# Optimization experiments

Measured on AMD Instinct MI355X. Metric: run time of the kernel, lower is better.

Reference implementation:

```python
import jax, jax.numpy as jnp
import numpy as np
from jax import lax

N, B, H, E = 50, 1024, 256, 256
FEA, SF = 8, 5
C_TANH = 10.0  # tanh_exploration, use_tanh=True for pointer


def setup_inputs() -> dict:
    key = jax.random.key(0)
    ks = iter(jax.random.split(key, 40))
    def rn(shape):
        return jax.random.normal(next(ks), shape, dtype=jnp.float32)
    def up(shape):
        s = 1.0 / np.sqrt(shape[-1])
        return jax.random.uniform(next(ks), shape, minval=-s, maxval=s, dtype=jnp.float32)
    inp = {
        'start_fea': rn((B, SF)),
        'decoder_input': rn((B, E)),
        'embedded_inputs': rn((N, B, E)),
        'hidden_h': rn((B, H)),
        'hidden_c': rn((B, H)),
        'context': rn((N, B, H)),
        'V': rn((B, N, FEA)),
        'V_reach_mask': jnp.zeros((B, N), dtype=bool),
        # LSTMCell (pointer decoder)
        'lstm_w_ih': up((4 * H, E)), 'lstm_w_hh': up((4 * H, H)),
        'lstm_b_ih': up((4 * H,)), 'lstm_b_hh': up((4 * H,)),
        # pointer attention
        'ptr_wq': up((H, H)), 'ptr_bq': up((H,)),
        'ptr_wr': up((H, H)), 'ptr_br': up((H,)), 'ptr_v': up((H,)),
        # glimpse attention
        'glp_wq': up((H, H)), 'glp_bq': up((H,)),
        'glp_wr': up((H, H)), 'glp_br': up((H,)), 'glp_v': up((H,)),
        # eta branch
        'fn_w': up((H, SF)),
        'eta_w_ih': up((4 * H, H)), 'eta_w_hh': up((4 * H, H)),
        'eta_b_ih': up((4 * H,)), 'eta_b_hh': up((4 * H,)),
        'eta_lin_w': up((1, 2 * H)), 'eta_lin_b': up((1,)),
    }
    return inp


def _lstm_cell(x, h, c, wi, wh, bi, bh):
    z = x @ wi.T + bi + h @ wh.T + bh
    i, f, g, o = jnp.split(z, 4, axis=1)  # torch chunk order i,f,g,o
    c2 = jax.nn.sigmoid(f) * c + jax.nn.sigmoid(i) * jnp.tanh(g)
    return jax.nn.sigmoid(o) * jnp.tanh(c2), c2


def _mask_modify(m):
    # if a row is all True, un-mask its last column
    return m.at[:, -1].set(jnp.where(m.all(axis=1), False, m[:, -1]))


def reference(start_fea, decoder_input, embedded_inputs, hidden_h, hidden_c,
              context, V, V_reach_mask,
              lstm_w_ih, lstm_w_hh, lstm_b_ih, lstm_b_hh,
              ptr_wq, ptr_bq, ptr_wr, ptr_br, ptr_v,
              glp_wq, glp_bq, glp_wr, glp_br, glp_v,
              fn_w, eta_w_ih, eta_w_hh, eta_b_ih, eta_b_hh,
              eta_lin_w, eta_lin_b):
    n_steps, bsz = embedded_inputs.shape[0], embedded_inputs.shape[1]
    barange = jnp.arange(bsz)
    # project_ref is a 1x1 conv over fixed context -> precompute once: [B,H,N]
    e_ptr = jnp.einsum('nbh,gh->bgn', context, ptr_wr) + ptr_br[None, :, None]
    e_glp = jnp.einsum('nbh,gh->bgn', context, glp_wr) + glp_br[None, :, None]

    def attn_logits(q_in, e, wq, bq, v):
        q = q_in @ wq.T + bq  # [B,H]
        return jnp.einsum('h,bhn->bn', v, jnp.tanh(q[:, :, None] + e))

    first_node = start_fea @ fn_w.T  # [B,H], no bias
    he, ce = _lstm_cell(first_node, hidden_h, hidden_c, eta_w_ih, eta_w_hh, eta_b_ih, eta_b_hh)
    mask0 = _mask_modify(V_reach_mask)

    def step(carry, step_i):
        h, c, mask, idxs, dec_in, heh, cec, last_node, cur_eta = carry
        upd = _mask_modify(mask.at[barange, idxs].set(True))
        logit_mask = jnp.where(step_i == 0, mask, upd)
        # pointer LSTM step
        h, c = _lstm_cell(dec_in, h, c, lstm_w_ih, lstm_w_hh, lstm_b_ih, lstm_b_hh)
        g_l = h
        # one glimpse (n_glimpses=1, mask_glimpses=True, use_tanh=False)
        u = attn_logits(g_l, e_glp, glp_wq, glp_bq, glp_v)
        u = jnp.where(logit_mask, -jnp.inf, u)
        g_l = jnp.einsum('bhn,bn->bh', e_glp, jax.nn.softmax(u, axis=1))
        # pointer (use_tanh=True, C=10, mask_logits=True)
        u = attn_logits(g_l, e_ptr, ptr_wq, ptr_bq, ptr_v)
        logits = jnp.where(logit_mask, -jnp.inf, C_TANH * jnp.tanh(u))
        log_p = jax.nn.log_softmax(logits, axis=1)  # [B,N]
        new_idxs = jnp.argmax(log_p, axis=1)  # greedy decode
        # eta branch
        cur_node = context[new_idxs, barange]  # [B,H]
        heh, cec = _lstm_cell(cur_node, heh, cec, eta_w_ih, eta_w_hh, eta_b_ih, eta_b_hh)
        eta = jnp.concatenate([last_node, cur_node], axis=1) @ eta_lin_w.T + eta_lin_b  # [B,1]
        cur_eta = cur_eta + eta
        dec_in2 = embedded_inputs[new_idxs, barange]  # [B,E]
        new_carry = (h, c, logit_mask, new_idxs, dec_in2, heh, cec, cur_node, cur_eta)
        return new_carry, (log_p, new_idxs, cur_eta[:, 0])

    init = (hidden_h, hidden_c, mask0, jnp.zeros((bsz,), jnp.int32), decoder_input,
            he, ce, first_node, jnp.zeros((bsz, 1), jnp.float32))
    _, (log_ps, sels, etas) = lax.scan(step, init, jnp.arange(n_steps))
    # stack along step dim -> [B, N, ...]
    return log_ps.transpose(1, 0, 2), sels.T, etas.T
```

## Files before the change

kernel.cpp:

```cpp
#include <hip/hip_runtime.h>
#include <hip/hip_bf16.h>

#define NSTEP 50
#define BSZ   1024
#define HD    256
#define RPB   4
#define NEG_INF (-__builtin_inff())

#define OFF_SEL ((size_t)BSZ * NSTEP * NSTEP)
#define OFF_ETA (OFF_SEL + (size_t)BSZ * NSTEP)

__device__ __forceinline__ float sigf(float x)      { return 1.f / (1.f + __expf(-x)); }
__device__ __forceinline__ float tanh_fast(float x) { return 1.f - 2.f / (__expf(2.f * x) + 1.f); }

__device__ __forceinline__ float wave_sum(float v) {
#pragma unroll
  for (int o = 1; o < 64; o <<= 1) v += __shfl_xor(v, o);
  return v;
}
__device__ __forceinline__ float wave_max(float v) {
#pragma unroll
  for (int o = 1; o < 64; o <<= 1) v = fmaxf(v, __shfl_xor(v, o));
  return v;
}

__global__ __launch_bounds__(256) void init_kernel(
    const float* __restrict__ w_ih, const float* __restrict__ w_hh,
    const float* __restrict__ b_ih, const float* __restrict__ b_hh,
    const float* __restrict__ glp_wq, const float* __restrict__ ptr_wq,
    float* __restrict__ wT2, float* __restrict__ bc,
    float* __restrict__ wqTg, float* __restrict__ wqTp)
{
  const int bid = blockIdx.x, tid = threadIdx.x;
  if (bid < 512) {
    const int k = bid;
    const float* src = (k < 256) ? (w_ih + k) : (w_hh + (k - 256));
#pragma unroll
    for (int g = 0; g < 4; ++g)
      wT2[(size_t)k * 1024 + tid * 4 + g] = src[(size_t)(g * 256 + tid) * 256];
  } else if (bid < 516) {
    const int j = (bid - 512) * 256 + tid;
    bc[j] = b_ih[j] + b_hh[j];
  } else {
    const int k = bid - 516;
    wqTg[(size_t)k * 256 + tid] = glp_wq[(size_t)tid * 256 + k];
    wqTp[(size_t)k * 256 + tid] = ptr_wq[(size_t)tid * 256 + k];
  }
}

__global__ __launch_bounds__(256) void e_kernel(
    const float* __restrict__ context,
    const float* __restrict__ glp_wr, const float* __restrict__ glp_br,
    const float* __restrict__ ptr_wr, const float* __restrict__ ptr_br,
    float* __restrict__ e_glp, float* __restrict__ e_ptr)
{
  __shared__ float ctx_lds[32][256];
  const int tid = threadIdx.x;
  const int n   = blockIdx.x >> 5;
  const int b0  = (blockIdx.x & 31) << 5;
  const float* src = context + ((size_t)n * BSZ + b0) * HD;
  for (int i = tid; i < 32 * 64; i += 256) {
    const int row = i >> 6, k4 = (i & 63) << 2;
    *(float4*)&ctx_lds[row][k4] = *(const float4*)&src[row * HD + k4];
  }
  __syncthreads();
  const int g  = tid;
  const float bg = glp_br[g], bp = ptr_br[g];
  for (int rg = 0; rg < 2; ++rg) {
    float ag[16], ap[16];
#pragma unroll
    for (int i = 0; i < 16; ++i) { ag[i] = 0.f; ap[i] = 0.f; }
    for (int k = 0; k < 256; k += 4) {
      float4 wg = *(const float4*)&glp_wr[g * HD + k];
      float4 wp = *(const float4*)&ptr_wr[g * HD + k];
#pragma unroll
      for (int i = 0; i < 16; ++i) {
        float4 a = *(const float4*)&ctx_lds[rg * 16 + i][k];
        ag[i] += a.x * wg.x + a.y * wg.y + a.z * wg.z + a.w * wg.w;
        ap[i] += a.x * wp.x + a.y * wp.y + a.z * wp.z + a.w * wp.w;
      }
    }
#pragma unroll
    for (int i = 0; i < 16; ++i) {
      const int b = b0 + rg * 16 + i;
      e_glp[((size_t)b * NSTEP + n) * HD + g] = ag[i] + bg;
      e_ptr[((size_t)b * NSTEP + n) * HD + g] = ap[i] + bp;
    }
  }
}

__global__ __launch_bounds__(256) void zx_kernel(
    const float* __restrict__ embedded, const float* __restrict__ decoder_input,
    const float* __restrict__ wT2, float* __restrict__ zx)
{
  __shared__ float x_lds[32][256];
  const int tid = threadIdx.x;
  const int n   = blockIdx.x >> 5;
  const int b0  = (blockIdx.x & 31) << 5;
  const float* src = (n < NSTEP) ? (embedded + ((size_t)n * BSZ + b0) * HD)
                                 : (decoder_input + (size_t)b0 * HD);
  for (int i = tid; i < 32 * 64; i += 256) {
    const int row = i >> 6, k4 = (i & 63) << 2;
    *(float4*)&x_lds[row][k4] = *(const float4*)&src[row * HD + k4];
  }
  __syncthreads();
  const float* wp = wT2 + (tid << 2);
  for (int rg = 0; rg < 2; ++rg) {
    float4 acc[16];
#pragma unroll
    for (int i = 0; i < 16; ++i) acc[i] = make_float4(0.f, 0.f, 0.f, 0.f);
    for (int k = 0; k < 256; k += 4) {
      float4 w0 = *(const float4*)(wp + (size_t)(k + 0) * 1024);
      float4 w1 = *(const float4*)(wp + (size_t)(k + 1) * 1024);
      float4 w2 = *(const float4*)(wp + (size_t)(k + 2) * 1024);
      float4 w3 = *(const float4*)(wp + (size_t)(k + 3) * 1024);
#pragma unroll
      for (int i = 0; i < 16; ++i) {
        float4 a = *(const float4*)&x_lds[rg * 16 + i][k];
        acc[i].x += a.x * w0.x + a.y * w1.x + a.z * w2.x + a.w * w3.x;
        acc[i].y += a.x * w0.y + a.y * w1.y + a.z * w2.y + a.w * w3.y;
        acc[i].z += a.x * w0.z + a.y * w1.z + a.z * w2.z + a.w * w3.z;
        acc[i].w += a.x * w0.w + a.y * w1.w + a.z * w2.w + a.w * w3.w;
      }
    }
#pragma unroll
    for (int i = 0; i < 16; ++i)
      *(float4*)&zx[((size_t)n * BSZ + (b0 + rg * 16 + i)) * 1024 + (tid << 2)] = acc[i];
  }
}

template <int PRE>
__global__ __launch_bounds__(512) void dec_kernel(
    const float* __restrict__ start_fea,
    const float* __restrict__ decoder_input,
    const float* __restrict__ embedded,
    const float* __restrict__ hidden_h,
    const float* __restrict__ hidden_c,
    const float* __restrict__ context,
    const unsigned char* __restrict__ vmask,
    const float* __restrict__ glp_bq, const float* __restrict__ glp_v,
    const float* __restrict__ ptr_bq, const float* __restrict__ ptr_v,
    const float* __restrict__ fn_w,
    const float* __restrict__ eta_lw, const float* __restrict__ eta_lb,
    const float* __restrict__ wT2, const float* __restrict__ bc,
    const float* __restrict__ wqTg, const float* __restrict__ wqTp,
    const float* __restrict__ e_glp, const float* __restrict__ e_ptr,
    const float* __restrict__ zx,
    float* __restrict__ out)
{
  __shared__ float a_lds[RPB][512];
  __shared__ float z_lds[RPB][1024];
  __shared__ float u_lds[RPB][52];
  __shared__ unsigned char mask_lds[RPB][64];
  __shared__ float ms_lds[RPB][2][2];
  __shared__ int   idx_lds[RPB];
  __shared__ float red_lds[8][2];
  __shared__ float eta_lds[RPB];

  const int tid  = threadIdx.x;
  const int col  = tid & 255;
  const int hf   = tid >> 8;
  const int wav  = tid >> 6;
  const int lane = tid & 63;
  const int b0   = blockIdx.x * RPB;
  const int r2   = hf * 2;
  const int cwr  = wav >> 1;
  const int cwh  = wav & 1;
  const int n0   = cwh * 25;
  const int k0   = hf << 7;

  float c_reg[2], ln_reg[2];

#pragma unroll
  for (int i2 = 0; i2 < 2; ++i2) {
    const int r = r2 + i2, b = b0 + r;
    a_lds[r][256 + col] = hidden_h[(size_t)b * HD + col];
    if (!PRE) a_lds[r][col] = decoder_input[(size_t)b * HD + col];
    c_reg[i2] = hidden_c[(size_t)b * HD + col];
    float fn = 0.f;
#pragma unroll
    for (int k = 0; k < 5; ++k) fn += start_fea[b * 5 + k] * fn_w[col * 5 + k];
    ln_reg[i2] = fn;
  }
  if (tid < RPB * NSTEP) {
    const int r = tid / NSTEP, n = tid - r * NSTEP;
    mask_lds[r][n] = vmask[(size_t)(b0 + r) * NSTEP + n];
  }
  if (tid < RPB) { eta_lds[tid] = 0.f; idx_lds[tid] = NSTEP; }
  __syncthreads();
  if (tid < RPB) {
    bool all = true;
    for (int n = 0; n < NSTEP; ++n) all = all && (mask_lds[tid][n] != 0);
    if (all) mask_lds[tid][NSTEP - 1] = 0;
  }
  __syncthreads();

  const float bch0 = bc[col], bch1 = bc[col + 256], bch2 = bc[col + 512], bch3 = bc[col + 768];
  const float lw0 = eta_lw[col], lw1 = eta_lw[HD + col];
  const float etaB = eta_lb[0];
  const float4 v4g  = *(const float4*)&glp_v[lane << 2];
  const float4 v4p  = *(const float4*)&ptr_v[lane << 2];
  const float4 v4bg = *(const float4*)&glp_bq[lane << 2];
  const float4 v4bp = *(const float4*)&ptr_bq[lane << 2];
  const int j2 = tid * 2;

  for (int t = 0; t < NSTEP; ++t) {
    {
      float2 acc[RPB];
      if (PRE) {
#pragma unroll
        for (int i = 0; i < RPB; ++i)
          acc[i] = *(const float2*)&zx[((size_t)idx_lds[i] * BSZ + (b0 + i)) * 1024 + j2];
      } else {
#pragma unroll
        for (int i = 0; i < RPB; ++i) acc[i] = make_float2(0.f, 0.f);
      }
      const int K0 = PRE ? 256 : 0;
      for (int k = K0; k < 512; k += 4) {
        float4 a4[RPB];
#pragma unroll
        for (int i = 0; i < RPB; ++i) a4[i] = *(const float4*)&a_lds[i][k];
        float2 w0 = *(const float2*)&wT2[(size_t)(k + 0) * 1024 + j2];
        float2 w1 = *(const float2*)&wT2[(size_t)(k + 1) * 1024 + j2];
        float2 w2 = *(const float2*)&wT2[(size_t)(k + 2) * 1024 + j2];
        float2 w3 = *(const float2*)&wT2[(size_t)(k + 3) * 1024 + j2];
#pragma unroll
        for (int i = 0; i < RPB; ++i) {
          acc[i].x += a4[i].x * w0.x + a4[i].y * w1.x + a4[i].z * w2.x + a4[i].w * w3.x;
          acc[i].y += a4[i].x * w0.y + a4[i].y * w1.y + a4[i].z * w2.y + a4[i].w * w3.y;
        }
      }
#pragma unroll
      for (int i = 0; i < RPB; ++i) *(float2*)&z_lds[i][j2] = acc[i];
    }
    __syncthreads();
#pragma unroll
    for (int i2 = 0; i2 < 2; ++i2) {
      const int r = r2 + i2;
      const float4 z4 = *(const float4*)&z_lds[r][col << 2];
      const float zi = z4.x + bch0, zf = z4.y + bch1, zg = z4.z + bch2, zo = z4.w + bch3;
      const float cn = sigf(zf) * c_reg[i2] + sigf(zi) * tanh_fast(zg);
      c_reg[i2] = cn;
      a_lds[r][256 + col] = sigf(zo) * tanh_fast(cn);
    }
    __syncthreads();
    {
      float accB[RPB] = {0.f, 0.f, 0.f, 0.f};
      for (int k = k0; k < k0 + 128; k += 4) {
        float4 a4[RPB];
#pragma unroll
        for (int i = 0; i < RPB; ++i) a4[i] = *(const float4*)&a_lds[i][256 + k];
        const float w0 = wqTg[(size_t)(k + 0) * 256 + col];
        const float w1 = wqTg[(size_t)(k + 1) * 256 + col];
        const float w2 = wqTg[(size_t)(k + 2) * 256 + col];
        const float w3 = wqTg[(size_t)(k + 3) * 256 + col];
#pragma unroll
        for (int i = 0; i < RPB; ++i)
          accB[i] += a4[i].x * w0 + a4[i].y * w1 + a4[i].z * w2 + a4[i].w * w3;
      }
#pragma unroll
      for (int i = 0; i < RPB; ++i) z_lds[i][(hf << 8) + col] = accB[i];
    }
    __syncthreads();
    {
      const int r = cwr, b = b0 + r;
      float4 q4;
      {
        const float4 p0 = *(const float4*)&z_lds[r][lane << 2];
        const float4 p1 = *(const float4*)&z_lds[r][256 + (lane << 2)];
        q4 = make_float4(p0.x + p1.x + v4bg.x, p0.y + p1.y + v4bg.y,
                         p0.z + p1.z + v4bg.z, p0.w + p1.w + v4bg.w);
      }
      float m = NEG_INF, s = 0.f;
      float4 G = make_float4(0.f, 0.f, 0.f, 0.f);
      const float* eb = e_glp + (size_t)b * NSTEP * HD;
      for (int n = n0; n < n0 + 25; ++n) {
        if (mask_lds[r][n]) continue;
        const float4 e4 = *(const float4*)&eb[n * HD + (lane << 2)];
        float uu = v4g.x * tanh_fast(q4.x + e4.x) + v4g.y * tanh_fast(q4.y + e4.y)
                 + v4g.z * tanh_fast(q4.z + e4.z) + v4g.w * tanh_fast(q4.w + e4.w);
        uu = wave_sum(uu);
        if (uu > m) {
          const float sc = __expf(m - uu);
          s *= sc; G.x *= sc; G.y *= sc; G.z *= sc; G.w *= sc;
          m = uu;
        }
        const float p = __expf(uu - m);
        s += p;
        G.x += p * e4.x; G.y += p * e4.y; G.z += p * e4.z; G.w += p * e4.w;
      }
      if (lane == 0) { ms_lds[r][cwh][0] = m; ms_lds[r][cwh][1] = s; }
      __syncthreads();
      const float mo = ms_lds[r][cwh ^ 1][0], so = ms_lds[r][cwh ^ 1][1];
      const float mg = fmaxf(m, mo);
      const float Z  = s * __expf(m - mg) + so * __expf(mo - mg);
      const float sc = __expf(m - mg) / Z;
      G.x *= sc; G.y *= sc; G.z *= sc; G.w *= sc;
      *(float4*)&z_lds[r][512 + (cwh << 8) + (lane << 2)] = G;
    }
    __syncthreads();
    {
      float accE[RPB] = {0.f, 0.f, 0.f, 0.f};
      for (int k = k0; k < k0 + 128; k += 4) {
        float4 g4[RPB];
#pragma unroll
        for (int i = 0; i < RPB; ++i) {
          const float4 ga = *(const float4*)&z_lds[i][512 + k];
          const float4 gb = *(const float4*)&z_lds[i][768 + k];
          g4[i] = make_float4(ga.x + gb.x, ga.y + gb.y, ga.z + gb.z, ga.w + gb.w);
        }
        const float w0 = wqTp[(size_t)(k + 0) * 256 + col];
        const float w1 = wqTp[(size_t)(k + 1) * 256 + col];
        const float w2 = wqTp[(size_t)(k + 2) * 256 + col];
        const float w3 = wqTp[(size_t)(k + 3) * 256 + col];
#pragma unroll
        for (int i = 0; i < RPB; ++i)
          accE[i] += g4[i].x * w0 + g4[i].y * w1 + g4[i].z * w2 + g4[i].w * w3;
      }
#pragma unroll
      for (int i = 0; i < RPB; ++i) z_lds[i][(hf << 8) + col] = accE[i];
    }
    __syncthreads();
    {
      const int r = cwr, b = b0 + r;
      float4 q4;
      {
        const float4 p0 = *(const float4*)&z_lds[r][lane << 2];
        const float4 p1 = *(const float4*)&z_lds[r][256 + (lane << 2)];
        q4 = make_float4(p0.x + p1.x + v4bp.x, p0.y + p1.y + v4bp.y,
                         p0.z + p1.z + v4bp.z, p0.w + p1.w + v4bp.w);
      }
      const float* eb = e_ptr + (size_t)b * NSTEP * HD;
      for (int n = n0; n < n0 + 25; ++n) {
        const float4 e4 = *(const float4*)&eb[n * HD + (lane << 2)];
        float uu = v4p.x * tanh_fast(q4.x + e4.x) + v4p.y * tanh_fast(q4.y + e4.y)
                 + v4p.z * tanh_fast(q4.z + e4.z) + v4p.w * tanh_fast(q4.w + e4.w);
        uu = wave_sum(uu);
        if (lane == 0) u_lds[r][n] = uu;
      }
    }
    __syncthreads();
    if (wav < RPB) {
      const int r = wav, b = b0 + r;
      const bool mk = (lane < NSTEP) ? (mask_lds[r][lane] != 0) : true;
      const float lg = mk ? NEG_INF : (10.f * tanh_fast(u_lds[r][lane]));
      const float m  = wave_max(lg);
      const float ex = (lane < NSTEP) ? __expf(lg - m) : 0.f;
      const float ss = wave_sum(ex);
      const float ls = __logf(ss);
      if (lane < NSTEP)
        out[(size_t)b * (NSTEP * NSTEP) + (size_t)t * NSTEP + lane] =
            mk ? -1.0e30f : ((lg - m) - ls);
      float av = lg;
      int   ai = lane;
#pragma unroll
      for (int o = 1; o < 64; o <<= 1) {
        const float ov = __shfl_xor(av, o);
        const int   oi = __shfl_xor(ai, o);
        if (ov > av || (ov == av && oi < ai)) { av = ov; ai = oi; }
      }
      if (lane == 0) {
        idx_lds[r] = ai;
        out[OFF_SEL + (size_t)b * NSTEP + t] = (float)ai;
      }
    }
    __syncthreads();
    {
      float pr[2];
#pragma unroll
      for (int i2 = 0; i2 < 2; ++i2) {
        const int r = r2 + i2, b = b0 + r;
        const int ix = idx_lds[r];
        const float cur = context[((size_t)ix * BSZ + b) * HD + col];
        pr[i2] = ln_reg[i2] * lw0 + cur * lw1;
        ln_reg[i2] = cur;
        if (!PRE) a_lds[r][col] = embedded[((size_t)ix * BSZ + b) * HD + col];
      }
#pragma unroll
      for (int o = 1; o < 64; o <<= 1) {
        pr[0] += __shfl_xor(pr[0], o);
        pr[1] += __shfl_xor(pr[1], o);
      }
      if (lane == 0) { red_lds[wav][0] = pr[0]; red_lds[wav][1] = pr[1]; }
    }
    __syncthreads();
    if (tid < RPB) {
      const int r = tid, hfr = r >> 1, i2 = r & 1;
      const float s = red_lds[hfr * 4 + 0][i2] + red_lds[hfr * 4 + 1][i2]
                    + red_lds[hfr * 4 + 2][i2] + red_lds[hfr * 4 + 3][i2];
      const float ev = eta_lds[r] + s + etaB;
      eta_lds[r] = ev;
      out[OFF_ETA + (size_t)(b0 + r) * NSTEP + t] = ev;
      const int ix = idx_lds[r];
      mask_lds[r][ix] = 1;
      bool all = true;
      for (int n = 0; n < NSTEP; ++n) all = all && (mask_lds[r][n] != 0);
      if (all) mask_lds[r][NSTEP - 1] = 0;
    }
    __syncthreads();
  }
}

extern "C" void kernel_launch(void* const* d_in, const int* in_sizes, int n_in,
                              void* d_out, int out_size, void* d_ws, size_t ws_size,
                              hipStream_t stream) {
  const float* start_fea  = (const float*)d_in[0];
  const float* decoder_in = (const float*)d_in[1];
  const float* embedded   = (const float*)d_in[2];
  const float* hidden_h   = (const float*)d_in[3];
  const float* hidden_c   = (const float*)d_in[4];
  const float* context    = (const float*)d_in[5];
  const unsigned char* vmask = (const unsigned char*)d_in[7];
  const float* lstm_w_ih  = (const float*)d_in[8];
  const float* lstm_w_hh  = (const float*)d_in[9];
  const float* lstm_b_ih  = (const float*)d_in[10];
  const float* lstm_b_hh  = (const float*)d_in[11];
  const float* ptr_wq     = (const float*)d_in[12];
  const float* ptr_bq     = (const float*)d_in[13];
  const float* ptr_wr     = (const float*)d_in[14];
  const float* ptr_br     = (const float*)d_in[15];
  const float* ptr_v      = (const float*)d_in[16];
  const float* glp_wq     = (const float*)d_in[17];
  const float* glp_bq     = (const float*)d_in[18];
  const float* glp_wr     = (const float*)d_in[19];
  const float* glp_br     = (const float*)d_in[20];
  const float* glp_v      = (const float*)d_in[21];
  const float* fn_w       = (const float*)d_in[22];
  const float* eta_lw     = (const float*)d_in[27];
  const float* eta_lb     = (const float*)d_in[28];

  float* ws    = (float*)d_ws;
  float* e_glp = ws;
  float* e_ptr = e_glp + (size_t)BSZ * NSTEP * HD;
  float* wT2   = e_ptr + (size_t)BSZ * NSTEP * HD;
  float* bc    = wT2 + (size_t)512 * 1024;
  float* wqTg  = bc + 1024;
  float* wqTp  = wqTg + 65536;
  float* zx    = wqTp + 65536;

  const size_t need_pre =
      ((size_t)BSZ * NSTEP * HD * 2 + (size_t)512 * 1024 + 1024 + 2 * 65536 +
       (size_t)(NSTEP + 1) * BSZ * 1024) * sizeof(float);
  const bool pre = (ws_size >= need_pre);

  init_kernel<<<772, 256, 0, stream>>>(lstm_w_ih, lstm_w_hh, lstm_b_ih, lstm_b_hh,
                                       glp_wq, ptr_wq, wT2, bc, wqTg, wqTp);
  e_kernel<<<NSTEP * 32, 256, 0, stream>>>(context, glp_wr, glp_br, ptr_wr, ptr_br, e_glp, e_ptr);
  if (pre) {
    zx_kernel<<<(NSTEP + 1) * 32, 256, 0, stream>>>(embedded, decoder_in, wT2, zx);
    dec_kernel<1><<<BSZ / RPB, 512, 0, stream>>>(
        start_fea, decoder_in, embedded, hidden_h, hidden_c, context, vmask,
        glp_bq, glp_v, ptr_bq, ptr_v, fn_w, eta_lw, eta_lb,
        wT2, bc, wqTg, wqTp, e_glp, e_ptr, zx, (float*)d_out);
  } else {
    dec_kernel<0><<<BSZ / RPB, 512, 0, stream>>>(
        start_fea, decoder_in, embedded, hidden_h, hidden_c, context, vmask,
        glp_bq, glp_v, ptr_bq, ptr_v, fn_w, eta_lw, eta_lb,
        wT2, bc, wqTg, wqTp, e_glp, e_ptr, zx, (float*)d_out);
  }
}
```

Before: 5.281 ms.

## Halve rows per block and split attention across four waves per row

Reduces rows per block from 4 to 2, doubling the block count so more blocks run per CU, and adds a launch-bounds occupancy hint. Each row's attention over the 50 nodes is now split across four waves instead of two, using a four-way online-softmax merge. A separate q_lds buffer holds query projections. The aim is more parallelism and latency hiding, at the cost of half the weight reuse per load and more total L2 weight traffic.

Measured after the change: 5.995 ms. 13.5% more time.

```diff
diff --git a/kernel.cpp b/kernel.cpp
--- a/kernel.cpp
+++ b/kernel.cpp
@@ -4,7 +4,7 @@
 #define NSTEP 50
 #define BSZ   1024
 #define HD    256
-#define RPB   4
+#define RPB   2
 #define NEG_INF (-__builtin_inff())
 
 #define OFF_SEL ((size_t)BSZ * NSTEP * NSTEP)
@@ -130,7 +130,7 @@
 }
 
 template <int PRE>
-__global__ __launch_bounds__(512) void dec_kernel(
+__global__ __launch_bounds__(512, 4) void dec_kernel(
     const float* __restrict__ start_fea,
     const float* __restrict__ decoder_input,
     const float* __restrict__ embedded,
@@ -150,11 +150,12 @@
 {
   __shared__ float a_lds[RPB][512];
   __shared__ float z_lds[RPB][1024];
+  __shared__ float q_lds[RPB][512];
   __shared__ float u_lds[RPB][52];
   __shared__ unsigned char mask_lds[RPB][64];
-  __shared__ float ms_lds[RPB][2][2];
+  __shared__ float ms_lds[RPB][4][2];
   __shared__ int   idx_lds[RPB];
-  __shared__ float red_lds[8][2];
+  __shared__ float red_lds[8];
   __shared__ float eta_lds[RPB];
 
   const int tid  = threadIdx.x;
@@ -163,24 +164,24 @@
   const int wav  = tid >> 6;
   const int lane = tid & 63;
   const int b0   = blockIdx.x * RPB;
-  const int r2   = hf * 2;
-  const int cwr  = wav >> 1;
-  const int cwh  = wav & 1;
-  const int n0   = cwh * 25;
+  const int cr   = wav >> 2;
+  const int cq   = wav & 3;
+  const int n0   = cq * 13;
+  const int n1   = (cq == 3) ? NSTEP : (n0 + 13);
   const int k0   = hf << 7;
-
-  float c_reg[2], ln_reg[2];
-
-#pragma unroll
-  for (int i2 = 0; i2 < 2; ++i2) {
-    const int r = r2 + i2, b = b0 + r;
+  const int j2   = tid * 2;
+
+  float c_reg, ln_reg;
+
+  {
+    const int r = hf, b = b0 + r;
     a_lds[r][256 + col] = hidden_h[(size_t)b * HD + col];
     if (!PRE) a_lds[r][col] = decoder_input[(size_t)b * HD + col];
-    c_reg[i2] = hidden_c[(size_t)b * HD + col];
+    c_reg = hidden_c[(size_t)b * HD + col];
     float fn = 0.f;
 #pragma unroll
     for (int k = 0; k < 5; ++k) fn += start_fea[b * 5 + k] * fn_w[col * 5 + k];
-    ln_reg[i2] = fn;
+    ln_reg = fn;
   }
   if (tid < RPB * NSTEP) {
     const int r = tid / NSTEP, n = tid - r * NSTEP;
@@ -202,7 +203,6 @@
   const float4 v4p  = *(const float4*)&ptr_v[lane << 2];
   const float4 v4bg = *(const float4*)&glp_bq[lane << 2];
   const float4 v4bp = *(const float4*)&ptr_bq[lane << 2];
-  const int j2 = tid * 2;
 
   for (int t = 0; t < NSTEP; ++t) {
     {
@@ -220,10 +220,10 @@
         float4 a4[RPB];
 #pragma unroll
         for (int i = 0; i < RPB; ++i) a4[i] = *(const float4*)&a_lds[i][k];
-        float2 w0 = *(const float2*)&wT2[(size_t)(k + 0) * 1024 + j2];
-        float2 w1 = *(const float2*)&wT2[(size_t)(k + 1) * 1024 + j2];
-        float2 w2 = *(const float2*)&wT2[(size_t)(k + 2) * 1024 + j2];
-        float2 w3 = *(const float2*)&wT2[(size_t)(k + 3) * 1024 + j2];
+        const float2 w0 = *(const float2*)&wT2[(size_t)(k + 0) * 1024 + j2];
+        const float2 w1 = *(const float2*)&wT2[(size_t)(k + 1) * 1024 + j2];
+        const float2 w2 = *(const float2*)&wT2[(size_t)(k + 2) * 1024 + j2];
+        const float2 w3 = *(const float2*)&wT2[(size_t)(k + 3) * 1024 + j2];
 #pragma unroll
         for (int i = 0; i < RPB; ++i) {
           acc[i].x += a4[i].x * w0.x + a4[i].y * w1.x + a4[i].z * w2.x + a4[i].w * w3.x;
@@ -234,18 +234,16 @@
       for (int i = 0; i < RPB; ++i) *(float2*)&z_lds[i][j2] = acc[i];
     }
     __syncthreads();
-#pragma unroll
-    for (int i2 = 0; i2 < 2; ++i2) {
-      const int r = r2 + i2;
-      const float4 z4 = *(const float4*)&z_lds[r][col << 2];
+    {
+      const float4 z4 = *(const float4*)&z_lds[hf][col << 2];
       const float zi = z4.x + bch0, zf = z4.y + bch1, zg = z4.z + bch2, zo = z4.w + bch3;
-      const float cn = sigf(zf) * c_reg[i2] + sigf(zi) * tanh_fast(zg);
-      c_reg[i2] = cn;
-      a_lds[r][256 + col] = sigf(zo) * tanh_fast(cn);
-    }
-    __syncthreads();
-    {
-      float accB[RPB] = {0.f, 0.f, 0.f, 0.f};
+      const float cn = sigf(zf) * c_reg + sigf(zi) * tanh_fast(zg);
+      c_reg = cn;
+      a_lds[hf][256 + col] = sigf(zo) * tanh_fast(cn);
+    }
+    __syncthreads();
+    {
+      float accB[RPB] = {0.f, 0.f};
       for (int k = k0; k < k0 + 128; k += 4) {
         float4 a4[RPB];
 #pragma unroll
@@ -259,22 +257,22 @@
           accB[i] += a4[i].x * w0 + a4[i].y * w1 + a4[i].z * w2 + a4[i].w * w3;
       }
 #pragma unroll
-      for (int i = 0; i < RPB; ++i) z_lds[i][(hf << 8) + col] = accB[i];
-    }
-    __syncthreads();
-    {
-      const int r = cwr, b = b0 + r;
+      for (int i = 0; i < RPB; ++i) q_lds[i][(hf << 8) + col] = accB[i];
+    }
+    __syncthreads();
+    {
+      const int r = cr, b = b0 + r;
       float4 q4;
       {
-        const float4 p0 = *(const float4*)&z_lds[r][lane << 2];
-        const float4 p1 = *(const float4*)&z_lds[r][256 + (lane << 2)];
+        const float4 p0 = *(const float4*)&q_lds[r][lane << 2];
+        const float4 p1 = *(const float4*)&q_lds[r][256 + (lane << 2)];
         q4 = make_float4(p0.x + p1.x + v4bg.x, p0.y + p1.y + v4bg.y,
                          p0.z + p1.z + v4bg.z, p0.w + p1.w + v4bg.w);
       }
       float m = NEG_INF, s = 0.f;
       float4 G = make_float4(0.f, 0.f, 0.f, 0.f);
       const float* eb = e_glp + (size_t)b * NSTEP * HD;
-      for (int n = n0; n < n0 + 25; ++n) {
+      for (int n = n0; n < n1; ++n) {
         if (mask_lds[r][n]) continue;
         const float4 e4 = *(const float4*)&eb[n * HD + (lane << 2)];
         float uu = v4g.x * tanh_fast(q4.x + e4.x) + v4g.y * tanh_fast(q4.y + e4.y)
@@ -289,25 +287,31 @@
         s += p;
         G.x += p * e4.x; G.y += p * e4.y; G.z += p * e4.z; G.w += p * e4.w;
       }
-      if (lane == 0) { ms_lds[r][cwh][0] = m; ms_lds[r][cwh][1] = s; }
+      if (lane == 0) { ms_lds[r][cq][0] = m; ms_lds[r][cq][1] = s; }
       __syncthreads();
-      const float mo = ms_lds[r][cwh ^ 1][0], so = ms_lds[r][cwh ^ 1][1];
-      const float mg = fmaxf(m, mo);
-      const float Z  = s * __expf(m - mg) + so * __expf(mo - mg);
+      float mg = NEG_INF;
+#pragma unroll
+      for (int q = 0; q < 4; ++q) mg = fmaxf(mg, ms_lds[r][q][0]);
+      float Z = 0.f;
+#pragma unroll
+      for (int q = 0; q < 4; ++q) Z += ms_lds[r][q][1] * __expf(ms_lds[r][q][0] - mg);
       const float sc = __expf(m - mg) / Z;
       G.x *= sc; G.y *= sc; G.z *= sc; G.w *= sc;
-      *(float4*)&z_lds[r][512 + (cwh << 8) + (lane << 2)] = G;
-    }
-    __syncthreads();
-    {
-      float accE[RPB] = {0.f, 0.f, 0.f, 0.f};
+      *(float4*)&z_lds[r][(cq << 8) + (lane << 2)] = G;
+    }
+    __syncthreads();
+    {
+      float accE[RPB] = {0.f, 0.f};
       for (int k = k0; k < k0 + 128; k += 4) {
         float4 g4[RPB];
 #pragma unroll
         for (int i = 0; i < RPB; ++i) {
-          const float4 ga = *(const float4*)&z_lds[i][512 + k];
-          const float4 gb = *(const float4*)&z_lds[i][768 + k];
-          g4[i] = make_float4(ga.x + gb.x, ga.y + gb.y, ga.z + gb.z, ga.w + gb.w);
+          const float4 g0 = *(const float4*)&z_lds[i][k];
+          const float4 g1 = *(const float4*)&z_lds[i][256 + k];
+          const float4 g2 = *(const float4*)&z_lds[i][512 + k];
+          const float4 g3 = *(const float4*)&z_lds[i][768 + k];
+          g4[i] = make_float4(g0.x + g1.x + g2.x + g3.x, g0.y + g1.y + g2.y + g3.y,
+                              g0.z + g1.z + g2.z + g3.z, g0.w + g1.w + g2.w + g3.w);
         }
         const float w0 = wqTp[(size_t)(k + 0) * 256 + col];
         const float w1 = wqTp[(size_t)(k + 1) * 256 + col];
@@ -318,20 +322,20 @@
           accE[i] += g4[i].x * w0 + g4[i].y * w1 + g4[i].z * w2 + g4[i].w * w3;
       }
 #pragma unroll
-      for (int i = 0; i < RPB; ++i) z_lds[i][(hf << 8) + col] = accE[i];
-    }
-    __syncthreads();
-    {
-      const int r = cwr, b = b0 + r;
+      for (int i = 0; i < RPB; ++i) q_lds[i][(hf << 8) + col] = accE[i];
+    }
+    __syncthreads();
+    {
+      const int r = cr, b = b0 + r;
       float4 q4;
       {
-        const float4 p0 = *(const float4*)&z_lds[r][lane << 2];
-        const float4 p1 = *(const float4*)&z_lds[r][256 + (lane << 2)];
+        const float4 p0 = *(const float4*)&q_lds[r][lane << 2];
+        const float4 p1 = *(const float4*)&q_lds[r][256 + (lane << 2)];
         q4 = make_float4(p0.x + p1.x + v4bp.x, p0.y + p1.y + v4bp.y,
                          p0.z + p1.z + v4bp.z, p0.w + p1.w + v4bp.w);
       }
       const float* eb = e_ptr + (size_t)b * NSTEP * HD;
-      for (int n = n0; n < n0 + 25; ++n) {
+      for (int n = n0; n < n1; ++n) {
         const float4 e4 = *(const float4*)&eb[n * HD + (lane << 2)];
         float uu = v4p.x * tanh_fast(q4.x + e4.x) + v4p.y * tanh_fast(q4.y + e4.y)
                  + v4p.z * tanh_fast(q4.z + e4.z) + v4p.w * tanh_fast(q4.w + e4.w);
@@ -366,28 +370,20 @@
     }
     __syncthreads();
     {
-      float pr[2];
-#pragma unroll
-      for (int i2 = 0; i2 < 2; ++i2) {
-        const int r = r2 + i2, b = b0 + r;
-        const int ix = idx_lds[r];
-        const float cur = context[((size_t)ix * BSZ + b) * HD + col];
-        pr[i2] = ln_reg[i2] * lw0 + cur * lw1;
-        ln_reg[i2] = cur;
-        if (!PRE) a_lds[r][col] = embedded[((size_t)ix * BSZ + b) * HD + col];
-      }
-#pragma unroll
-      for (int o = 1; o < 64; o <<= 1) {
-        pr[0] += __shfl_xor(pr[0], o);
-        pr[1] += __shfl_xor(pr[1], o);
-      }
-      if (lane == 0) { red_lds[wav][0] = pr[0]; red_lds[wav][1] = pr[1]; }
+      const int r = hf, b = b0 + r;
+      const int ix = idx_lds[r];
+      const float cur = context[((size_t)ix * BSZ + b) * HD + col];
+      float pr = ln_reg * lw0 + cur * lw1;
+      ln_reg = cur;
+      if (!PRE) a_lds[r][col] = embedded[((size_t)ix * BSZ + b) * HD + col];
+      pr = wave_sum(pr);
+      if (lane == 0) red_lds[wav] = pr;
     }
     __syncthreads();
     if (tid < RPB) {
-      const int r = tid, hfr = r >> 1, i2 = r & 1;
-      const float s = red_lds[hfr * 4 + 0][i2] + red_lds[hfr * 4 + 1][i2]
-                    + red_lds[hfr * 4 + 2][i2] + red_lds[hfr * 4 + 3][i2];
+      const int r = tid;
+      const float s = red_lds[r * 4 + 0] + red_lds[r * 4 + 1]
+                    + red_lds[r * 4 + 2] + red_lds[r * 4 + 3];
       const float ev = eta_lds[r] + s + etaB;
       eta_lds[r] = ev;
       out[OFF_ETA + (size_t)(b0 + r) * NSTEP + t] = ev;
```

## Transpose attention projections to per-node layout and parallelize attention over nodes

Applied to the files above, without the earlier changes.

Replaces the e_kernel with a per-batch et_kernel that stores the reference projections transposed as [B,H,N] and pre-scaled by 2, so the tanh folds into a single exp. In the decoder, each lane now handles one node and loops over the hidden dimension, replacing per-node wave reductions and the online softmax with one masked softmax and a separate weighted-sum pass. It also drops the precomputed zx input projection and computes the full 512-wide LSTM matmul every step. This trades extra per-step matmul work and strided global reads of the transposed projections for fewer cross-lane reductions and less serialization.

After: 9.690 ms. 83.5% more time.

```diff
diff --git a/kernel.cpp b/kernel.cpp
--- a/kernel.cpp
+++ b/kernel.cpp
@@ -48,88 +48,36 @@
   }
 }
 
-__global__ __launch_bounds__(256) void e_kernel(
+__global__ __launch_bounds__(256) void et_kernel(
     const float* __restrict__ context,
-    const float* __restrict__ glp_wr, const float* __restrict__ glp_br,
-    const float* __restrict__ ptr_wr, const float* __restrict__ ptr_br,
-    float* __restrict__ e_glp, float* __restrict__ e_ptr)
+    const float* __restrict__ wr, const float* __restrict__ br,
+    float* __restrict__ et)
 {
-  __shared__ float ctx_lds[32][256];
-  const int tid = threadIdx.x;
-  const int n   = blockIdx.x >> 5;
-  const int b0  = (blockIdx.x & 31) << 5;
-  const float* src = context + ((size_t)n * BSZ + b0) * HD;
-  for (int i = tid; i < 32 * 64; i += 256) {
-    const int row = i >> 6, k4 = (i & 63) << 2;
-    *(float4*)&ctx_lds[row][k4] = *(const float4*)&src[row * HD + k4];
+  __shared__ float c_lds[50][260];
+  const int b = blockIdx.x, tid = threadIdx.x;
+  for (int i = tid; i < 50 * 256; i += 256) {
+    const int n = i >> 8, k = i & 255;
+    c_lds[n][k] = context[((size_t)n * BSZ + b) * HD + k];
   }
   __syncthreads();
-  const int g  = tid;
-  const float bg = glp_br[g], bp = ptr_br[g];
-  for (int rg = 0; rg < 2; ++rg) {
-    float ag[16], ap[16];
-#pragma unroll
-    for (int i = 0; i < 16; ++i) { ag[i] = 0.f; ap[i] = 0.f; }
-    for (int k = 0; k < 256; k += 4) {
-      float4 wg = *(const float4*)&glp_wr[g * HD + k];
-      float4 wp = *(const float4*)&ptr_wr[g * HD + k];
-#pragma unroll
-      for (int i = 0; i < 16; ++i) {
-        float4 a = *(const float4*)&ctx_lds[rg * 16 + i][k];
-        ag[i] += a.x * wg.x + a.y * wg.y + a.z * wg.z + a.w * wg.w;
-        ap[i] += a.x * wp.x + a.y * wp.y + a.z * wp.z + a.w * wp.w;
-      }
-    }
-#pragma unroll
-    for (int i = 0; i < 16; ++i) {
-      const int b = b0 + rg * 16 + i;
-      e_glp[((size_t)b * NSTEP + n) * HD + g] = ag[i] + bg;
-      e_ptr[((size_t)b * NSTEP + n) * HD + g] = ap[i] + bp;
-    }
-  }
-}
-
-__global__ __launch_bounds__(256) void zx_kernel(
-    const float* __restrict__ embedded, const float* __restrict__ decoder_input,
-    const float* __restrict__ wT2, float* __restrict__ zx)
-{
-  __shared__ float x_lds[32][256];
-  const int tid = threadIdx.x;
-  const int n   = blockIdx.x >> 5;
-  const int b0  = (blockIdx.x & 31) << 5;
-  const float* src = (n < NSTEP) ? (embedded + ((size_t)n * BSZ + b0) * HD)
-                                 : (decoder_input + (size_t)b0 * HD);
-  for (int i = tid; i < 32 * 64; i += 256) {
-    const int row = i >> 6, k4 = (i & 63) << 2;
-    *(float4*)&x_lds[row][k4] = *(const float4*)&src[row * HD + k4];
-  }
-  __syncthreads();
-  const float* wp = wT2 + (tid << 2);
-  for (int rg = 0; rg < 2; ++rg) {
-    float4 acc[16];
-#pragma unroll
-    for (int i = 0; i < 16; ++i) acc[i] = make_float4(0.f, 0.f, 0.f, 0.f);
-    for (int k = 0; k < 256; k += 4) {
-      float4 w0 = *(const float4*)(wp + (size_t)(k + 0) * 1024);
-      float4 w1 = *(const float4*)(wp + (size_t)(k + 1) * 1024);
-      float4 w2 = *(const float4*)(wp + (size_t)(k + 2) * 1024);
-      float4 w3 = *(const float4*)(wp + (size_t)(k + 3) * 1024);
-#pragma unroll
-      for (int i = 0; i < 16; ++i) {
-        float4 a = *(const float4*)&x_lds[rg * 16 + i][k];
-        acc[i].x += a.x * w0.x + a.y * w1.x + a.z * w2.x + a.w * w3.x;
-        acc[i].y += a.x * w0.y + a.y * w1.y + a.z * w2.y + a.w * w3.y;
-        acc[i].z += a.x * w0.z + a.y * w1.z + a.z * w2.z + a.w * w3.z;
-        acc[i].w += a.x * w0.w + a.y * w1.w + a.z * w2.w + a.w * w3.w;
-      }
-    }
-#pragma unroll
-    for (int i = 0; i < 16; ++i)
-      *(float4*)&zx[((size_t)n * BSZ + (b0 + rg * 16 + i)) * 1024 + (tid << 2)] = acc[i];
-  }
-}
-
-template <int PRE>
+  float acc[50];
+#pragma unroll
+  for (int n = 0; n < 50; ++n) acc[n] = 0.f;
+  const float* wrh = wr + (size_t)tid * HD;
+  for (int k4 = 0; k4 < 64; ++k4) {
+    const float4 w4 = *(const float4*)&wrh[k4 * 4];
+#pragma unroll
+    for (int n = 0; n < 50; ++n) {
+      const float4 c4 = *(const float4*)&c_lds[n][k4 * 4];
+      acc[n] += c4.x * w4.x + c4.y * w4.y + c4.z * w4.z + c4.w * w4.w;
+    }
+  }
+  const float bb = br[tid];
+  float* dst = et + ((size_t)b * HD + tid) * NSTEP;
+#pragma unroll
+  for (int n = 0; n < 50; ++n) dst[n] = 2.f * (acc[n] + bb);
+}
+
 __global__ __launch_bounds__(512) void dec_kernel(
     const float* __restrict__ start_fea,
     const float* __restrict__ decoder_input,
@@ -144,15 +92,16 @@
     const float* __restrict__ eta_lw, const float* __restrict__ eta_lb,
     const float* __restrict__ wT2, const float* __restrict__ bc,
     const float* __restrict__ wqTg, const float* __restrict__ wqTp,
-    const float* __restrict__ e_glp, const float* __restrict__ e_ptr,
-    const float* __restrict__ zx,
+    const float* __restrict__ et_glp, const float* __restrict__ et_ptr,
     float* __restrict__ out)
 {
   __shared__ float a_lds[RPB][512];
   __shared__ float z_lds[RPB][1024];
-  __shared__ float u_lds[RPB][52];
+  __shared__ float qf_lds[RPB][256];
+  __shared__ float up_lds[RPB][2][64];
+  __shared__ float p_lds[RPB][64];
+  __shared__ float vv_lds[2][256];
   __shared__ unsigned char mask_lds[RPB][64];
-  __shared__ float ms_lds[RPB][2][2];
   __shared__ int   idx_lds[RPB];
   __shared__ float red_lds[8][2];
   __shared__ float eta_lds[RPB];
@@ -163,30 +112,30 @@
   const int wav  = tid >> 6;
   const int lane = tid & 63;
   const int b0   = blockIdx.x * RPB;
-  const int r2   = hf * 2;
-  const int cwr  = wav >> 1;
-  const int cwh  = wav & 1;
-  const int n0   = cwh * 25;
   const int k0   = hf << 7;
+  const int j2   = tid * 2;
+  const int cr   = wav >> 1;
+  const int ch   = wav & 1;
 
   float c_reg[2], ln_reg[2];
 
 #pragma unroll
-  for (int i2 = 0; i2 < 2; ++i2) {
-    const int r = r2 + i2, b = b0 + r;
+  for (int rr = 0; rr < 2; ++rr) {
+    const int r = hf * 2 + rr, b = b0 + r;
+    a_lds[r][col]       = decoder_input[(size_t)b * HD + col];
     a_lds[r][256 + col] = hidden_h[(size_t)b * HD + col];
-    if (!PRE) a_lds[r][col] = decoder_input[(size_t)b * HD + col];
-    c_reg[i2] = hidden_c[(size_t)b * HD + col];
+    c_reg[rr] = hidden_c[(size_t)b * HD + col];
     float fn = 0.f;
 #pragma unroll
     for (int k = 0; k < 5; ++k) fn += start_fea[b * 5 + k] * fn_w[col * 5 + k];
-    ln_reg[i2] = fn;
-  }
+    ln_reg[rr] = fn;
+  }
+  if (hf == 0) vv_lds[0][col] = glp_v[col]; else vv_lds[1][col] = ptr_v[col];
   if (tid < RPB * NSTEP) {
     const int r = tid / NSTEP, n = tid - r * NSTEP;
     mask_lds[r][n] = vmask[(size_t)(b0 + r) * NSTEP + n];
   }
-  if (tid < RPB) { eta_lds[tid] = 0.f; idx_lds[tid] = NSTEP; }
+  if (tid < RPB) { eta_lds[tid] = 0.f; idx_lds[tid] = 0; }
   __syncthreads();
   if (tid < RPB) {
     bool all = true;
@@ -198,32 +147,21 @@
   const float bch0 = bc[col], bch1 = bc[col + 256], bch2 = bc[col + 512], bch3 = bc[col + 768];
   const float lw0 = eta_lw[col], lw1 = eta_lw[HD + col];
   const float etaB = eta_lb[0];
-  const float4 v4g  = *(const float4*)&glp_v[lane << 2];
-  const float4 v4p  = *(const float4*)&ptr_v[lane << 2];
-  const float4 v4bg = *(const float4*)&glp_bq[lane << 2];
-  const float4 v4bp = *(const float4*)&ptr_bq[lane << 2];
-  const int j2 = tid * 2;
+  const float bqg = glp_bq[col], bqp = ptr_bq[col];
 
   for (int t = 0; t < NSTEP; ++t) {
     {
       float2 acc[RPB];
-      if (PRE) {
-#pragma unroll
-        for (int i = 0; i < RPB; ++i)
-          acc[i] = *(const float2*)&zx[((size_t)idx_lds[i] * BSZ + (b0 + i)) * 1024 + j2];
-      } else {
-#pragma unroll
-        for (int i = 0; i < RPB; ++i) acc[i] = make_float2(0.f, 0.f);
-      }
-      const int K0 = PRE ? 256 : 0;
-      for (int k = K0; k < 512; k += 4) {
+#pragma unroll
+      for (int i = 0; i < RPB; ++i) acc[i] = make_float2(0.f, 0.f);
+      for (int k = 0; k < 512; k += 4) {
         float4 a4[RPB];
 #pragma unroll
         for (int i = 0; i < RPB; ++i) a4[i] = *(const float4*)&a_lds[i][k];
-        float2 w0 = *(const float2*)&wT2[(size_t)(k + 0) * 1024 + j2];
-        float2 w1 = *(const float2*)&wT2[(size_t)(k + 1) * 1024 + j2];
-        float2 w2 = *(const float2*)&wT2[(size_t)(k + 2) * 1024 + j2];
-        float2 w3 = *(const float2*)&wT2[(size_t)(k + 3) * 1024 + j2];
+        const float2 w0 = *(const float2*)&wT2[(size_t)(k + 0) * 1024 + j2];
+        const float2 w1 = *(const float2*)&wT2[(size_t)(k + 1) * 1024 + j2];
+        const float2 w2 = *(const float2*)&wT2[(size_t)(k + 2) * 1024 + j2];
+        const float2 w3 = *(const float2*)&wT2[(size_t)(k + 3) * 1024 + j2];
 #pragma unroll
         for (int i = 0; i < RPB; ++i) {
           acc[i].x += a4[i].x * w0.x + a4[i].y * w1.x + a4[i].z * w2.x + a4[i].w * w3.x;
@@ -235,12 +173,12 @@
     }
     __syncthreads();
 #pragma unroll
-    for (int i2 = 0; i2 < 2; ++i2) {
-      const int r = r2 + i2;
+    for (int rr = 0; rr < 2; ++rr) {
+      const int r = hf * 2 + rr;
       const float4 z4 = *(const float4*)&z_lds[r][col << 2];
       const float zi = z4.x + bch0, zf = z4.y + bch1, zg = z4.z + bch2, zo = z4.w + bch3;
-      const float cn = sigf(zf) * c_reg[i2] + sigf(zi) * tanh_fast(zg);
-      c_reg[i2] = cn;
+      const float cn = sigf(zf) * c_reg[rr] + sigf(zi) * tanh_fast(zg);
+      c_reg[rr] = cn;
       a_lds[r][256 + col] = sigf(zo) * tanh_fast(cn);
     }
     __syncthreads();
@@ -262,41 +200,50 @@
       for (int i = 0; i < RPB; ++i) z_lds[i][(hf << 8) + col] = accB[i];
     }
     __syncthreads();
-    {
-      const int r = cwr, b = b0 + r;
-      float4 q4;
-      {
-        const float4 p0 = *(const float4*)&z_lds[r][lane << 2];
-        const float4 p1 = *(const float4*)&z_lds[r][256 + (lane << 2)];
-        q4 = make_float4(p0.x + p1.x + v4bg.x, p0.y + p1.y + v4bg.y,
-                         p0.z + p1.z + v4bg.z, p0.w + p1.w + v4bg.w);
-      }
-      float m = NEG_INF, s = 0.f;
-      float4 G = make_float4(0.f, 0.f, 0.f, 0.f);
-      const float* eb = e_glp + (size_t)b * NSTEP * HD;
-      for (int n = n0; n < n0 + 25; ++n) {
-        if (mask_lds[r][n]) continue;
-        const float4 e4 = *(const float4*)&eb[n * HD + (lane << 2)];
-        float uu = v4g.x * tanh_fast(q4.x + e4.x) + v4g.y * tanh_fast(q4.y + e4.y)
-                 + v4g.z * tanh_fast(q4.z + e4.z) + v4g.w * tanh_fast(q4.w + e4.w);
-        uu = wave_sum(uu);
-        if (uu > m) {
-          const float sc = __expf(m - uu);
-          s *= sc; G.x *= sc; G.y *= sc; G.z *= sc; G.w *= sc;
-          m = uu;
-        }
-        const float p = __expf(uu - m);
-        s += p;
-        G.x += p * e4.x; G.y += p * e4.y; G.z += p * e4.z; G.w += p * e4.w;
-      }
-      if (lane == 0) { ms_lds[r][cwh][0] = m; ms_lds[r][cwh][1] = s; }
-      __syncthreads();
-      const float mo = ms_lds[r][cwh ^ 1][0], so = ms_lds[r][cwh ^ 1][1];
-      const float mg = fmaxf(m, mo);
-      const float Z  = s * __expf(m - mg) + so * __expf(mo - mg);
-      const float sc = __expf(m - mg) / Z;
-      G.x *= sc; G.y *= sc; G.z *= sc; G.w *= sc;
-      *(float4*)&z_lds[r][512 + (cwh << 8) + (lane << 2)] = G;
+#pragma unroll
+    for (int rr = 0; rr < 2; ++rr) {
+      const int r = hf * 2 + rr;
+      qf_lds[r][col] = 2.f * (z_lds[r][col] + z_lds[r][256 + col] + bqg);
+    }
+    __syncthreads();
+    {
+      const int r = cr, b = b0 + r;
+      const float* et = et_glp + ((size_t)b * HD + (ch << 7)) * NSTEP + lane;
+      const float* qf = &qf_lds[r][ch << 7];
+      const float* vv = &vv_lds[0][ch << 7];
+      float u = 0.f;
+#pragma unroll 4
+      for (int h = 0; h < 128; ++h) {
+        const float x2 = qf[h] + et[h * NSTEP];
+        const float th = 1.f - 2.f / (__expf(x2) + 1.f);
+        u = fmaf(vv[h], th, u);
+      }
+      up_lds[r][ch][lane] = u;
+    }
+    __syncthreads();
+    if (wav < RPB) {
+      const int r = wav;
+      const bool mk = (lane < NSTEP) ? (mask_lds[r][lane] != 0) : true;
+      const float u = up_lds[r][0][lane] + up_lds[r][1][lane];
+      const float uv = mk ? NEG_INF : u;
+      const float m  = wave_max(uv);
+      const float ex = mk ? 0.f : __expf(uv - m);
+      const float ss = wave_sum(ex);
+      p_lds[r][lane] = 0.5f * (ex / ss);
+    }
+    __syncthreads();
+#pragma unroll
+    for (int rr = 0; rr < 2; ++rr) {
+      const int r = hf * 2 + rr, b = b0 + r;
+      const float2* eb = (const float2*)(et_glp + ((size_t)b * HD + col) * NSTEP);
+      float acc = 0.f;
+#pragma unroll
+      for (int q = 0; q < 25; ++q) {
+        const float2 e2 = eb[q];
+        const float2 p2 = *(const float2*)&p_lds[r][q * 2];
+        acc += e2.x * p2.x + e2.y * p2.y;
+      }
+      z_lds[r][col] = acc;
     }
     __syncthreads();
     {
@@ -304,11 +251,7 @@
       for (int k = k0; k < k0 + 128; k += 4) {
         float4 g4[RPB];
 #pragma unroll
-        for (int i = 0; i < RPB; ++i) {
-          const float4 ga = *(const float4*)&z_lds[i][512 + k];
-          const float4 gb = *(const float4*)&z_lds[i][768 + k];
-          g4[i] = make_float4(ga.x + gb.x, ga.y + gb.y, ga.z + gb.z, ga.w + gb.w);
-        }
+        for (int i = 0; i < RPB; ++i) g4[i] = *(const float4*)&z_lds[i][k];
         const float w0 = wqTp[(size_t)(k + 0) * 256 + col];
         const float w1 = wqTp[(size_t)(k + 1) * 256 + col];
         const float w2 = wqTp[(size_t)(k + 2) * 256 + col];
@@ -318,34 +261,37 @@
           accE[i] += g4[i].x * w0 + g4[i].y * w1 + g4[i].z * w2 + g4[i].w * w3;
       }
 #pragma unroll
-      for (int i = 0; i < RPB; ++i) z_lds[i][(hf << 8) + col] = accE[i];
-    }
-    __syncthreads();
-    {
-      const int r = cwr, b = b0 + r;
-      float4 q4;
-      {
-        const float4 p0 = *(const float4*)&z_lds[r][lane << 2];
-        const float4 p1 = *(const float4*)&z_lds[r][256 + (lane << 2)];
-        q4 = make_float4(p0.x + p1.x + v4bp.x, p0.y + p1.y + v4bp.y,
-                         p0.z + p1.z + v4bp.z, p0.w + p1.w + v4bp.w);
-      }
-      const float* eb = e_ptr + (size_t)b * NSTEP * HD;
-      for (int n = n0; n < n0 + 25; ++n) {
-        const float4 e4 = *(const float4*)&eb[n * HD + (lane << 2)];
-        float uu = v4p.x * tanh_fast(q4.x + e4.x) + v4p.y * tanh_fast(q4.y + e4.y)
-                 + v4p.z * tanh_fast(q4.z + e4.z) + v4p.w * tanh_fast(q4.w + e4.w);
-        uu = wave_sum(uu);
-        if (lane == 0) u_lds[r][n] = uu;
-      }
+      for (int i = 0; i < RPB; ++i) z_lds[i][512 + (hf << 8) + col] = accE[i];
+    }
+    __syncthreads();
+#pragma unroll
+    for (int rr = 0; rr < 2; ++rr) {
+      const int r = hf * 2 + rr;
+      qf_lds[r][col] = 2.f * (z_lds[r][512 + col] + z_lds[r][768 + col] + bqp);
+    }
+    __syncthreads();
+    {
+      const int r = cr, b = b0 + r;
+      const float* et = et_ptr + ((size_t)b * HD + (ch << 7)) * NSTEP + lane;
+      const float* qf = &qf_lds[r][ch << 7];
+      const float* vv = &vv_lds[1][ch << 7];
+      float u = 0.f;
+#pragma unroll 4
+      for (int h = 0; h < 128; ++h) {
+        const float x2 = qf[h] + et[h * NSTEP];
+        const float th = 1.f - 2.f / (__expf(x2) + 1.f);
+        u = fmaf(vv[h], th, u);
+      }
+      up_lds[r][ch][lane] = u;
     }
     __syncthreads();
     if (wav < RPB) {
       const int r = wav, b = b0 + r;
       const bool mk = (lane < NSTEP) ? (mask_lds[r][lane] != 0) : true;
-      const float lg = mk ? NEG_INF : (10.f * tanh_fast(u_lds[r][lane]));
+      const float u = up_lds[r][0][lane] + up_lds[r][1][lane];
+      const float lg = mk ? NEG_INF : (10.f * tanh_fast(u));
       const float m  = wave_max(lg);
-      const float ex = (lane < NSTEP) ? __expf(lg - m) : 0.f;
+      const float ex = mk ? 0.f : __expf(lg - m);
       const float ss = wave_sum(ex);
       const float ls = __logf(ss);
       if (lane < NSTEP)
@@ -368,13 +314,13 @@
     {
       float pr[2];
 #pragma unroll
-      for (int i2 = 0; i2 < 2; ++i2) {
-        const int r = r2 + i2, b = b0 + r;
+      for (int rr = 0; rr < 2; ++rr) {
+        const int r = hf * 2 + rr, b = b0 + r;
         const int ix = idx_lds[r];
         const float cur = context[((size_t)ix * BSZ + b) * HD + col];
-        pr[i2] = ln_reg[i2] * lw0 + cur * lw1;
-        ln_reg[i2] = cur;
-        if (!PRE) a_lds[r][col] = embedded[((size_t)ix * BSZ + b) * HD + col];
+        pr[rr] = ln_reg[rr] * lw0 + cur * lw1;
+        ln_reg[rr] = cur;
+        a_lds[r][col] = embedded[((size_t)ix * BSZ + b) * HD + col];
       }
 #pragma unroll
       for (int o = 1; o < 64; o <<= 1) {
@@ -385,9 +331,10 @@
     }
     __syncthreads();
     if (tid < RPB) {
-      const int r = tid, hfr = r >> 1, i2 = r & 1;
-      const float s = red_lds[hfr * 4 + 0][i2] + red_lds[hfr * 4 + 1][i2]
-                    + red_lds[hfr * 4 + 2][i2] + red_lds[hfr * 4 + 3][i2];
+      const int r = tid;
+      const int w0 = (r >> 1) * 4, rr = r & 1;
+      const float s = red_lds[w0][rr] + red_lds[w0 + 1][rr]
+                    + red_lds[w0 + 2][rr] + red_lds[w0 + 3][rr];
       const float ev = eta_lds[r] + s + etaB;
       eta_lds[r] = ev;
       out[OFF_ETA + (size_t)(b0 + r) * NSTEP + t] = ev;
@@ -429,33 +376,20 @@
   const float* eta_lw     = (const float*)d_in[27];
   const float* eta_lb     = (const float*)d_in[28];
 
-  float* ws    = (float*)d_ws;
-  float* e_glp = ws;
-  float* e_ptr = e_glp + (size_t)BSZ * NSTEP * HD;
-  float* wT2   = e_ptr + (size_t)BSZ * NSTEP * HD;
-  float* bc    = wT2 + (size_t)512 * 1024;
-  float* wqTg  = bc + 1024;
-  float* wqTp  = wqTg + 65536;
-  float* zx    = wqTp + 65536;
-
-  const size_t need_pre =
-      ((size_t)BSZ * NSTEP * HD * 2 + (size_t)512 * 1024 + 1024 + 2 * 65536 +
-       (size_t)(NSTEP + 1) * BSZ * 1024) * sizeof(float);
-  const bool pre = (ws_size >= need_pre);
+  float* ws     = (float*)d_ws;
+  float* wT2    = ws;
+  float* bc     = wT2 + (size_t)512 * 1024;
+  float* wqTg   = bc + 1024;
+  float* wqTp   = wqTg + 65536;
+  float* et_glp = wqTp + 65536;
+  float* et_ptr = et_glp + (size_t)BSZ * HD * NSTEP + 64;
 
   init_kernel<<<772, 256, 0, stream>>>(lstm_w_ih, lstm_w_hh, lstm_b_ih, lstm_b_hh,
                                        glp_wq, ptr_wq, wT2, bc, wqTg, wqTp);
-  e_kernel<<<NSTEP * 32, 256, 0, stream>>>(context, glp_wr, glp_br, ptr_wr, ptr_br, e_glp, e_ptr);
-  if (pre) {
-    zx_kernel<<<(NSTEP + 1) * 32, 256, 0, stream>>>(embedded, decoder_in, wT2, zx);
-    dec_kernel<1><<<BSZ / RPB, 512, 0, stream>>>(
-        start_fea, decoder_in, embedded, hidden_h, hidden_c, context, vmask,
-        glp_bq, glp_v, ptr_bq, ptr_v, fn_w, eta_lw, eta_lb,
-        wT2, bc, wqTg, wqTp, e_glp, e_ptr, zx, (float*)d_out);
-  } else {
-    dec_kernel<0><<<BSZ / RPB, 512, 0, stream>>>(
-        start_fea, decoder_in, embedded, hidden_h, hidden_c, context, vmask,
-        glp_bq, glp_v, ptr_bq, ptr_v, fn_w, eta_lw, eta_lb,
-        wT2, bc, wqTg, wqTp, e_glp, e_ptr, zx, (float*)d_out);
-  }
-}
+  et_kernel<<<BSZ, 256, 0, stream>>>(context, glp_wr, glp_br, et_glp);
+  et_kernel<<<BSZ, 256, 0, stream>>>(context, ptr_wr, ptr_br, et_ptr);
+  dec_kernel<<<BSZ / RPB, 512, 0, stream>>>(
+      start_fea, decoder_in, embedded, hidden_h, hidden_c, context, vmask,
+      glp_bq, glp_v, ptr_bq, ptr_v, fn_w, eta_lw, eta_lb,
+      wT2, bc, wqTg, wqTp, et_glp, et_ptr, (float*)d_out);
+}
```
